# Optimization experiments

Measured on AMD Instinct MI355X. Metric: run time of the kernel, lower is better.

Reference implementation:

```python
import jax, jax.numpy as jnp
import numpy as np

B, S, H, I, G = 2, 1024, 1024, 4096, 8


def setup_inputs() -> dict:
    key = jax.random.key(0)
    k1, k2, k3, k4 = jax.random.split(key, 4)
    # kaiming-style scaled init (scale matters only for numerics, not math)
    hidden_states = jax.random.normal(k1, (B, S, H), dtype=jnp.float32)
    WG = jax.random.normal(k2, (H, G), dtype=jnp.float32) * (1.0 / np.sqrt(H))
    Wi = jax.random.normal(k3, (G, H, I), dtype=jnp.float32) * (1.0 / np.sqrt(H))
    down = jax.random.normal(k4, (I, H), dtype=jnp.float32) * (1.0 / np.sqrt(I))
    return {"hidden_states": hidden_states, "WG": WG, "Wi": Wi, "down": down, "topk": 2}


def topk_sigmoid(gate, k):
    # gate: [B,S,G] -> sigmoid gated scores masked to top-k per token
    _, idx = jax.lax.top_k(gate, k)                       # idx: [B,S,k]
    mask = (idx[..., None] == jnp.arange(gate.shape[-1])).any(axis=-2)  # [B,S,G] bool
    return jax.nn.sigmoid(gate) * mask


def reference(hidden_states, WG, Wi, down, topk):
    gate = hidden_states @ WG                             # [B,S,G]
    g = topk_sigmoid(gate, topk)                          # [B,S,G]
    # dense contraction over all groups (faithful to original einsum)
    up = jnp.einsum('bse,bsg,geo->bso', hidden_states, g, Wi)  # [B,S,I]
    act = jnp.square(jax.nn.relu(up))                     # ReLU^2
    return act @ down                                     # [B,S,H]
```

## Files before the change

kernel.cpp:

```cpp
#include <hip/hip_runtime.h>
#include <hip/hip_bf16.h>

typedef unsigned short u16;
typedef short short8_t __attribute__((ext_vector_type(8)));
typedef float f32x4 __attribute__((ext_vector_type(4)));

#define GLOBAL_AS(p) ((const __attribute__((address_space(1))) void*)(p))
#define LDS_AS(p)    ((__attribute__((address_space(3))) void*)(p))

__device__ __forceinline__ u16 f2bf(float f) {
    union { float f; unsigned int u; } x;
    x.f = f;
    unsigned int r = x.u + 0x7fffu + ((x.u >> 16) & 1u);
    return (u16)(r >> 16);
}

#define M_NMT   0
#define M_TE    2
#define M_TB    42
#define M_PAIR  96
#define M_RTOK  4192
#define M_RW    9312

__global__ __launch_bounds__(64) void gate_topk_kernel(
    const float* __restrict__ h, const float* __restrict__ wg, float* __restrict__ w) {
    const int t = blockIdx.x;
    const int lane = threadIdx.x;
    float acc[8];
#pragma unroll
    for (int g = 0; g < 8; ++g) acc[g] = 0.f;
    for (int e = lane; e < 1024; e += 64) {
        float hv = h[(size_t)t * 1024 + e];
        float4 r0 = *(const float4*)&wg[e * 8];
        float4 r1 = *(const float4*)&wg[e * 8 + 4];
        acc[0] += hv * r0.x; acc[1] += hv * r0.y; acc[2] += hv * r0.z; acc[3] += hv * r0.w;
        acc[4] += hv * r1.x; acc[5] += hv * r1.y; acc[6] += hv * r1.z; acc[7] += hv * r1.w;
    }
#pragma unroll
    for (int off = 32; off > 0; off >>= 1) {
#pragma unroll
        for (int g = 0; g < 8; ++g) acc[g] += __shfl_down(acc[g], off);
    }
    if (lane == 0) {
        int i1 = 0;
        for (int g = 1; g < 8; ++g) if (acc[g] > acc[i1]) i1 = g;
        int i2 = -1;
        for (int g = 0; g < 8; ++g) {
            if (g == i1) continue;
            if (i2 < 0 || acc[g] > acc[i2]) i2 = g;
        }
#pragma unroll
        for (int g = 0; g < 8; ++g) {
            float v = (g == i1 || g == i2) ? (1.f / (1.f + __expf(-acc[g]))) : 0.f;
            w[t * 8 + g] = v;
        }
    }
}

__global__ __launch_bounds__(256) void scan_kernel(
    const float* __restrict__ w, int* __restrict__ meta) {
    __shared__ int cnt[8], pos[8];
    const int tid = threadIdx.x;
    if (tid < 8) cnt[tid] = 0;
    __syncthreads();
    for (int t = tid; t < 2048; t += 256) {
#pragma unroll
        for (int g = 0; g < 8; ++g)
            if (w[t * 8 + g] > 0.f) atomicAdd(&cnt[g], 1);
    }
    __syncthreads();
    if (tid == 0) {
        int base = 0, mt = 0;
        for (int e = 0; e < 8; ++e) {
            pos[e] = base;
            int nt = (cnt[e] + 127) >> 7;
            for (int k = 0; k < nt; ++k) { meta[M_TE + mt] = e; meta[M_TB + mt] = base + k * 128; ++mt; }
            base += nt << 7;
        }
        meta[M_NMT] = mt;
        meta[1] = base;
    }
    __syncthreads();
    for (int i = tid; i < 5120; i += 256) meta[M_RTOK + i] = -1;
    __syncthreads();
    float* row_w = (float*)&meta[M_RW];
    for (int t = tid; t < 2048; t += 256) {
        int slot = 0;
#pragma unroll
        for (int g = 0; g < 8; ++g) {
            float wv = w[t * 8 + g];
            if (wv > 0.f) {
                int p = atomicAdd(&pos[g], 1);
                meta[M_RTOK + p] = t;
                row_w[p] = wv;
                meta[M_PAIR + t * 2 + slot] = p;
                ++slot;
            }
        }
    }
}

__global__ __launch_bounds__(256) void gather_a_kernel(
    const float* __restrict__ h, const int* __restrict__ meta, u16* __restrict__ A) {
    const int row = blockIdx.x;
    const int tid = threadIdx.x;
    const int tok = meta[M_RTOK + row];
    u16* dst = A + (size_t)row * 1024;
    if (tok < 0) {
        uint2 z; z.x = 0u; z.y = 0u;
        ((uint2*)dst)[tid] = z;
        return;
    }
    const float wv = ((const float*)&meta[M_RW])[row];
    float4 v = ((const float4*)(h + (size_t)tok * 1024))[tid];
    u16 o[4] = { f2bf(v.x * wv), f2bf(v.y * wv), f2bf(v.z * wv), f2bf(v.w * wv) };
    ((uint2*)dst)[tid] = *(const uint2*)o;
}

__global__ __launch_bounds__(256) void gemm1_sparse_kernel(
    const u16* __restrict__ A, const float* __restrict__ Wi,
    float* __restrict__ up, const int* __restrict__ meta) {
    const int mt = blockIdx.y;
    if (mt >= meta[M_NMT]) return;
    const int e = meta[M_TE + mt];
    const int base = meta[M_TB + mt];
    const int n0 = blockIdx.x * 128;
    const int K = 1024, N = 4096;
    const float* Bm = Wi + (size_t)e * K * N;

    __shared__ short a_tile[128 * 64];
    __shared__ short b_tile[128 * 64];
    const int tid = threadIdx.x;
    const int lane = tid & 63;
    const int wave = tid >> 6;
    const int wm = (wave >> 1) * 64;
    const int wn = (wave & 1) * 64;
    const int r = lane & 15;
    const int quad = lane >> 4;
    const int rowin = lane >> 3;
    const int achk = ((lane & 7) ^ (rowin & 7)) * 8;
    const int aldst = (lane & 7) * 8;

    const int bidx_n = tid & 127;
    const int bidx_k8 = tid >> 7;

    const f32x4 vzero = {0.f, 0.f, 0.f, 0.f};
    f32x4 acc[4][4];
#pragma unroll
    for (int i = 0; i < 4; ++i)
#pragma unroll
        for (int j = 0; j < 4; ++j) acc[i][j] = vzero;

    float bv[4][8];
#pragma unroll
    for (int cb = 0; cb < 4; ++cb) {
        const float* bp = Bm + (size_t)((bidx_k8 + cb * 2) * 8) * N + n0 + bidx_n;
#pragma unroll
        for (int kk = 0; kk < 8; ++kk) bv[cb][kk] = bp[(size_t)kk * N];
    }

    for (int kb = 0; kb < K; kb += 64) {
#pragma unroll
        for (int it = 0; it < 4; ++it) {
            int row = wave * 8 + it * 32 + rowin;
            const u16* ga = A + (size_t)(base + row) * K + kb + achk;
            __builtin_amdgcn_global_load_lds(GLOBAL_AS(ga), LDS_AS(&a_tile[row * 64 + aldst]), 16, 0, 0);
        }
#pragma unroll
        for (int cb = 0; cb < 4; ++cb) {
            int bk8 = bidx_k8 + cb * 2;
            u16 bc[8];
#pragma unroll
            for (int kk = 0; kk < 8; ++kk) bc[kk] = f2bf(bv[cb][kk]);
            *(short8_t*)&b_tile[bidx_n * 64 + ((bk8 ^ (bidx_n & 7)) * 8)] = *(const short8_t*)bc;
        }
        __syncthreads();

        if (kb + 64 < K) {
#pragma unroll
            for (int cb = 0; cb < 4; ++cb) {
                const float* bp = Bm + (size_t)(kb + 64 + (bidx_k8 + cb * 2) * 8) * N + n0 + bidx_n;
#pragma unroll
                for (int kk = 0; kk < 8; ++kk) bv[cb][kk] = bp[(size_t)kk * N];
            }
        }

#pragma unroll
        for (int ks = 0; ks < 2; ++ks) {
            const int cp = ((ks * 4 + quad) ^ (r & 7)) * 8;
            short8_t af[4], bfr[4];
#pragma unroll
            for (int i = 0; i < 4; ++i)
                af[i] = *(const short8_t*)&a_tile[(wm + i * 16 + r) * 64 + cp];
#pragma unroll
            for (int j = 0; j < 4; ++j)
                bfr[j] = *(const short8_t*)&b_tile[(wn + j * 16 + r) * 64 + cp];
#pragma unroll
            for (int i = 0; i < 4; ++i)
#pragma unroll
                for (int j = 0; j < 4; ++j)
                    acc[i][j] = __builtin_amdgcn_mfma_f32_16x16x32_bf16(af[i], bfr[j], acc[i][j], 0, 0, 0);
        }
        __syncthreads();
    }
#pragma unroll
    for (int i = 0; i < 4; ++i)
#pragma unroll
        for (int j = 0; j < 4; ++j)
#pragma unroll
            for (int reg = 0; reg < 4; ++reg) {
                int cr = base + wm + i * 16 + quad * 4 + reg;
                int cc = n0 + wn + j * 16 + r;
                up[(size_t)cr * N + cc] = acc[i][j][reg];
            }
}

__global__ __launch_bounds__(256) void combine_kernel(
    const float* __restrict__ up, const int* __restrict__ meta, u16* __restrict__ act) {
    const int t = blockIdx.x;
    const int tid = threadIdx.x;
    const int p0 = meta[M_PAIR + t * 2];
    const int p1 = meta[M_PAIR + t * 2 + 1];
    const float* r0 = up + (size_t)p0 * 4096;
    const float* r1 = up + (size_t)p1 * 4096;
    u16* dst = act + (size_t)t * 4096;
#pragma unroll
    for (int it = 0; it < 4; ++it) {
        int i = (tid + it * 256) * 4;
        float4 a = *(const float4*)&r0[i];
        float4 b = *(const float4*)&r1[i];
        float s0 = a.x + b.x, s1 = a.y + b.y, s2 = a.z + b.z, s3 = a.w + b.w;
        s0 = s0 > 0.f ? s0 * s0 : 0.f;
        s1 = s1 > 0.f ? s1 * s1 : 0.f;
        s2 = s2 > 0.f ? s2 * s2 : 0.f;
        s3 = s3 > 0.f ? s3 * s3 : 0.f;
        u16 o[4] = { f2bf(s0), f2bf(s1), f2bf(s2), f2bf(s3) };
        *(uint2*)&dst[i] = *(const uint2*)o;
    }
}

__global__ __launch_bounds__(256) void transpose_cvt_kernel(
    const float* __restrict__ in, u16* __restrict__ out, int R, int C) {
    __shared__ u16 tile[64][65];
    const int rt = blockIdx.y * 64;
    const int ct = blockIdx.x * 64;
    const int tid = threadIdx.x;
#pragma unroll
    for (int it = 0; it < 2; ++it) {
        int r = (tid >> 3) + it * 32;
        int c8 = (tid & 7) * 8;
        const float* ip = &in[(size_t)(rt + r) * C + ct + c8];
        float4 v0 = *(const float4*)ip;
        float4 v1 = *(const float4*)(ip + 4);
        tile[c8 + 0][r] = f2bf(v0.x); tile[c8 + 1][r] = f2bf(v0.y);
        tile[c8 + 2][r] = f2bf(v0.z); tile[c8 + 3][r] = f2bf(v0.w);
        tile[c8 + 4][r] = f2bf(v1.x); tile[c8 + 5][r] = f2bf(v1.y);
        tile[c8 + 6][r] = f2bf(v1.z); tile[c8 + 7][r] = f2bf(v1.w);
    }
    __syncthreads();
#pragma unroll
    for (int it = 0; it < 2; ++it) {
        int c = (tid >> 3) + it * 32;
        int r8 = (tid & 7) * 8;
        u16 tmp[8];
#pragma unroll
        for (int j = 0; j < 8; ++j) tmp[j] = tile[c][r8 + j];
        *(uint4*)&out[(size_t)(ct + c) * R + rt + r8] = *(const uint4*)tmp;
    }
}

template <int BM, int WROWS, int WCOLS>
__global__ __launch_bounds__(256) void gemm_tn_kernel(
    const u16* __restrict__ X, const u16* __restrict__ Y, float* __restrict__ Cout,
    int M, int N, int K) {
    constexpr int WM = BM / WROWS;
    constexpr int WN = 128 / WCOLS;
    constexpr int FI = WM / 16;
    constexpr int FJ = WN / 16;
    __shared__ short a_tile[BM * 64];
    __shared__ short b_tile[128 * 64];
    const int tid = threadIdx.x;
    const int lane = tid & 63;
    const int wave = tid >> 6;

    const int Nt = gridDim.x, Mt = gridDim.y;
    const int lid = blockIdx.y * Nt + blockIdx.x;
    const int xcd = lid & 7;
    const int p = lid >> 3;
    const int n_tile = xcd * (Nt >> 3) + p / Mt;
    const int m_tile = p % Mt;
    const int m0 = m_tile * BM;
    const int n0 = n_tile * 128;

    const int wm = (wave / WCOLS) * WM;
    const int wn = (wave % WCOLS) * WN;
    const int rowin = lane >> 3;
    const int achk = ((lane & 7) ^ (rowin & 7)) * 8;
    const int aldst = (lane & 7) * 8;
    const int r = lane & 15;
    const int quad = lane >> 4;

    const f32x4 vzero = {0.f, 0.f, 0.f, 0.f};
    f32x4 acc[FI][FJ];
#pragma unroll
    for (int i = 0; i < FI; ++i)
#pragma unroll
        for (int j = 0; j < FJ; ++j) acc[i][j] = vzero;

    for (int kb = 0; kb < K; kb += 64) {
#pragma unroll
        for (int it = 0; it < BM / 32; ++it) {
            int row = wave * 8 + it * 32 + rowin;
            const u16* ga = X + (size_t)(m0 + row) * K + kb + achk;
            __builtin_amdgcn_global_load_lds(GLOBAL_AS(ga), LDS_AS(&a_tile[row * 64 + aldst]), 16, 0, 0);
        }
#pragma unroll
        for (int it = 0; it < 4; ++it) {
            int row = wave * 8 + it * 32 + rowin;
            const u16* gb = Y + (size_t)(n0 + row) * K + kb + achk;
            __builtin_amdgcn_global_load_lds(GLOBAL_AS(gb), LDS_AS(&b_tile[row * 64 + aldst]), 16, 0, 0);
        }
        __syncthreads();
#pragma unroll
        for (int ks = 0; ks < 2; ++ks) {
            const int cp = ((ks * 4 + quad) ^ (r & 7)) * 8;
            short8_t af[FI], bfr[FJ];
#pragma unroll
            for (int i = 0; i < FI; ++i)
                af[i] = *(const short8_t*)&a_tile[(wm + i * 16 + r) * 64 + cp];
#pragma unroll
            for (int j = 0; j < FJ; ++j)
                bfr[j] = *(const short8_t*)&b_tile[(wn + j * 16 + r) * 64 + cp];
#pragma unroll
            for (int i = 0; i < FI; ++i)
#pragma unroll
                for (int j = 0; j < FJ; ++j)
                    acc[i][j] = __builtin_amdgcn_mfma_f32_16x16x32_bf16(af[i], bfr[j], acc[i][j], 0, 0, 0);
        }
        __syncthreads();
    }
#pragma unroll
    for (int i = 0; i < FI; ++i)
#pragma unroll
        for (int j = 0; j < FJ; ++j)
#pragma unroll
            for (int reg = 0; reg < 4; ++reg) {
                int cr = m0 + wm + i * 16 + quad * 4 + reg;
                int cc = n0 + wn + j * 16 + r;
                Cout[(size_t)cr * N + cc] = acc[i][j][reg];
            }
}

extern "C" void kernel_launch(void* const* d_in, const int* in_sizes, int n_in,
                              void* d_out, int out_size, void* d_ws, size_t ws_size,
                              hipStream_t stream) {
    const float* h    = (const float*)d_in[0];
    const float* WG   = (const float*)d_in[1];
    const float* Wi   = (const float*)d_in[2];
    const float* down = (const float*)d_in[3];
    float* out = (float*)d_out;

    const int T = 2048, H = 1024, I = 4096;

    char* ws = (char*)d_ws;
    float* w_gate = (float*)(ws);
    int*   meta   = (int*)(ws + 65536);
    u16*   Arow   = (u16*)(ws + 131072);
    float* up     = (float*)(ws + 131072 + 10485760);
    u16*   act    = (u16*)(ws + 131072 + 10485760 + 83886080);
    u16*   downT  = (u16*)(ws + 131072 + 10485760 + 83886080 + 16777216);

    gate_topk_kernel<<<T, 64, 0, stream>>>(h, WG, w_gate);
    scan_kernel<<<1, 256, 0, stream>>>(w_gate, meta);
    gather_a_kernel<<<5120, 256, 0, stream>>>(h, meta, Arow);

    gemm1_sparse_kernel<<<dim3(32, 40), 256, 0, stream>>>(Arow, Wi, up, meta);

    combine_kernel<<<T, 256, 0, stream>>>(up, meta, act);

    transpose_cvt_kernel<<<dim3(H / 64, I / 64), 256, 0, stream>>>(down, downT, I, H);
    gemm_tn_kernel<64, 1, 4><<<dim3(H / 128, T / 64), 256, 0, stream>>>(
        act, downT, out, T, H, I);
}
```

Baseline: 373.4 us.

## Double-buffer LDS tiles in down-projection GEMM and halve M tile

Converts the down-projection GEMM's K loop to a two-stage LDS double buffer. The next tile's global-to-LDS loads are issued before the MFMAs on the current tile, so there is one barrier per iteration instead of two. The launch also switches to a 32-row M tile, doubling the grid to 512 blocks for better CU occupancy, at the cost of reloading the B operand more often. The double buffer doubles LDS use per block.

```diff
diff --git a/kernel.cpp b/kernel.cpp
--- a/kernel.cpp
+++ b/kernel.cpp
@@ -277,8 +277,8 @@
     constexpr int WN = 128 / WCOLS;
     constexpr int FI = WM / 16;
     constexpr int FJ = WN / 16;
-    __shared__ short a_tile[BM * 64];
-    __shared__ short b_tile[128 * 64];
+    __shared__ short a_tile[2][BM * 64];
+    __shared__ short b_tile[2][128 * 64];
     const int tid = threadIdx.x;
     const int lane = tid & 63;
     const int wave = tid >> 6;
@@ -307,38 +307,60 @@
 #pragma unroll
         for (int j = 0; j < FJ; ++j) acc[i][j] = vzero;
 
-    for (int kb = 0; kb < K; kb += 64) {
-#pragma unroll
-        for (int it = 0; it < BM / 32; ++it) {
-            int row = wave * 8 + it * 32 + rowin;
-            const u16* ga = X + (size_t)(m0 + row) * K + kb + achk;
-            __builtin_amdgcn_global_load_lds(GLOBAL_AS(ga), LDS_AS(&a_tile[row * 64 + aldst]), 16, 0, 0);
-        }
-#pragma unroll
-        for (int it = 0; it < 4; ++it) {
-            int row = wave * 8 + it * 32 + rowin;
-            const u16* gb = Y + (size_t)(n0 + row) * K + kb + achk;
-            __builtin_amdgcn_global_load_lds(GLOBAL_AS(gb), LDS_AS(&b_tile[row * 64 + aldst]), 16, 0, 0);
-        }
+#define G2_STAGE(kb_, buf)                                                            \
+    {                                                                                 \
+        const int kbc = (kb_);                                                        \
+        _Pragma("unroll")                                                             \
+        for (int it = 0; it < BM / 32; ++it) {                                        \
+            int row = wave * 8 + it * 32 + rowin;                                     \
+            const u16* ga = X + (size_t)(m0 + row) * K + kbc + achk;                  \
+            __builtin_amdgcn_global_load_lds(GLOBAL_AS(ga),                           \
+                LDS_AS(&a_tile[buf][row * 64 + aldst]), 16, 0, 0);                    \
+        }                                                                             \
+        _Pragma("unroll")                                                             \
+        for (int it = 0; it < 4; ++it) {                                              \
+            int row = wave * 8 + it * 32 + rowin;                                     \
+            const u16* gb = Y + (size_t)(n0 + row) * K + kbc + achk;                  \
+            __builtin_amdgcn_global_load_lds(GLOBAL_AS(gb),                           \
+                LDS_AS(&b_tile[buf][row * 64 + aldst]), 16, 0, 0);                    \
+        }                                                                             \
+    }
+
+#define G2_COMPUTE(buf)                                                               \
+    {                                                                                 \
+        _Pragma("unroll")                                                             \
+        for (int ks = 0; ks < 2; ++ks) {                                              \
+            const int cp = ((ks * 4 + quad) ^ (r & 7)) * 8;                           \
+            short8_t af[FI], bfr[FJ];                                                 \
+            _Pragma("unroll")                                                         \
+            for (int i = 0; i < FI; ++i)                                              \
+                af[i] = *(const short8_t*)&a_tile[buf][(wm + i * 16 + r) * 64 + cp];  \
+            _Pragma("unroll")                                                         \
+            for (int j = 0; j < FJ; ++j)                                              \
+                bfr[j] = *(const short8_t*)&b_tile[buf][(wn + j * 16 + r) * 64 + cp]; \
+            _Pragma("unroll")                                                         \
+            for (int i = 0; i < FI; ++i)                                              \
+                _Pragma("unroll")                                                     \
+                for (int j = 0; j < FJ; ++j)                                          \
+                    acc[i][j] = __builtin_amdgcn_mfma_f32_16x16x32_bf16(              \
+                        af[i], bfr[j], acc[i][j], 0, 0, 0);                           \
+        }                                                                             \
+    }
+
+    const int nk = K >> 6;
+    G2_STAGE(0, 0);
+    __syncthreads();
+    for (int t = 0; t < nk - 1; ++t) {
+        const int nxt = (t + 1) & 1;
+        G2_STAGE((t + 1) * 64, nxt);
+        G2_COMPUTE(t & 1);
         __syncthreads();
-#pragma unroll
-        for (int ks = 0; ks < 2; ++ks) {
-            const int cp = ((ks * 4 + quad) ^ (r & 7)) * 8;
-            short8_t af[FI], bfr[FJ];
-#pragma unroll
-            for (int i = 0; i < FI; ++i)
-                af[i] = *(const short8_t*)&a_tile[(wm + i * 16 + r) * 64 + cp];
-#pragma unroll
-            for (int j = 0; j < FJ; ++j)
-                bfr[j] = *(const short8_t*)&b_tile[(wn + j * 16 + r) * 64 + cp];
-#pragma unroll
-            for (int i = 0; i < FI; ++i)
-#pragma unroll
-                for (int j = 0; j < FJ; ++j)
-                    acc[i][j] = __builtin_amdgcn_mfma_f32_16x16x32_bf16(af[i], bfr[j], acc[i][j], 0, 0, 0);
-        }
-        __syncthreads();
-    }
+    }
+    G2_COMPUTE((nk - 1) & 1);
+
+#undef G2_STAGE
+#undef G2_COMPUTE
+
 #pragma unroll
     for (int i = 0; i < FI; ++i)
 #pragma unroll
@@ -379,6 +401,6 @@
     combine_kernel<<<T, 256, 0, stream>>>(up, meta, act);
 
     transpose_cvt_kernel<<<dim3(H / 64, I / 64), 256, 0, stream>>>(down, downT, I, H);
-    gemm_tn_kernel<64, 1, 4><<<dim3(H / 128, T / 64), 256, 0, stream>>>(
+    gemm_tn_kernel<32, 1, 4><<<dim3(H / 128, T / 32), 256, 0, stream>>>(
         act, downT, out, T, H, I);
 }
```

New measurement: 357.7 us. -4.2%, faster.
